# Kernel optimization log

Hardware: AMD Instinct MI355X
Metric: run time of the kernel (lower is better)

Reference implementation:

```python
import jax, jax.numpy as jnp
import numpy as np

B, P, DV, DT, E, A, K = 256, 192, 768, 768, 256, 8, 4


def _l2n(x):
    return x / jnp.maximum(jnp.linalg.norm(x, axis=-1, keepdims=True), 1e-12)


def _hungarian_min(cost):
    """Jonker-Volgenant style Hungarian (e-maxx formulation), minimizes cost.
    cost: [n, m] with n <= m. Returns (row_ind, col_ind) like scipy's
    linear_sum_assignment."""
    cost = np.asarray(cost, dtype=np.float64)
    n, m = cost.shape
    INF = 1e18
    u = np.zeros(n + 1)
    v = np.zeros(m + 1)
    p = np.zeros(m + 1, dtype=np.int64)   # p[j] = row matched to col j (1-based)
    way = np.zeros(m + 1, dtype=np.int64)
    for i in range(1, n + 1):
        p[0] = i
        j0 = 0
        minv = np.full(m + 1, INF)
        used = np.zeros(m + 1, dtype=bool)
        while True:
            used[j0] = True
            i0 = p[j0]
            cur = cost[i0 - 1] - u[i0] - v[1:]
            free = ~used[1:]
            better = free & (cur < minv[1:])
            minv[1:][better] = cur[better]
            way[1:][better] = j0
            cand = np.where(free, minv[1:], INF)
            j1 = int(np.argmin(cand)) + 1
            delta = cand[j1 - 1]
            u[p[used]] += delta
            v[used] -= delta
            minv[1:][free] -= delta
            j0 = j1
            if p[j0] == 0:
                break
        while j0 != 0:
            j1 = way[j0]
            p[j0] = p[j1]
            j0 = j1
    rows = p[1:]
    cols = np.arange(m)
    sel = rows != 0
    rows = rows[sel] - 1
    cols = cols[sel]
    order = np.argsort(rows)
    return rows[order], cols[order]


def _topk_assign_indices(sim_np, k):
    """Replicates get_topk_assign_similarity's iterative masked re-assignment,
    returning per-round match indices. sim_np: [B, A, P] numpy."""
    b_, a_, _ = sim_np.shape
    rows = np.zeros((k, b_, a_), dtype=np.int64)
    cols = np.zeros((k, b_, a_), dtype=np.int64)
    for b in range(b_):
        mat = sim_np[b].copy()
        for r in range(k):
            ri, ci = _hungarian_min(-mat)  # maximize similarity
            rows[r, b] = ri
            cols[r, b] = ci
            mat[ri, ci] = -100.0
        # (host loop over small per-sample Hungarian solves; this is exactly
        #  the serialized pattern the original module exhibits)
    return rows, cols


def setup_inputs() -> dict:
    key = jax.random.key(0)
    ks = jax.random.split(key, 8)
    s = (2.0 / E) ** 0.5  # kaiming_normal fan_out on [E, in] torch weight
    return {
        "visual_feature": jax.random.normal(ks[0], (B, 1 + P, DV), jnp.float32),
        "textual_feature": jax.random.normal(ks[1], (B, DT), jnp.float32),
        "attribute_feature": jax.random.normal(ks[2], (B * A, DT), jnp.float32),
        "att_nums": jnp.full((B,), A, dtype=jnp.int32),
        "Wv": jax.random.normal(ks[3], (DV, E), jnp.float32) * s,
        "bv": jnp.zeros((E,), jnp.float32),
        "Wt": jax.random.normal(ks[4], (DT, E), jnp.float32) * s,
        "bt": jnp.zeros((E,), jnp.float32),
        "Wp": jax.random.normal(ks[5], (DV, E), jnp.float32) * s,
        "bp": jnp.zeros((E,), jnp.float32),
        "Wa": jax.random.normal(ks[6], (DT, E), jnp.float32) * s,
        "ba": jnp.zeros((E,), jnp.float32),
    }


def reference(visual_feature, textual_feature, attribute_feature, att_nums,
              Wv, bv, Wt, bt, Wp, bp, Wa, ba):
    # ViT path: avgpool is None; split CLS token / patch tokens
    visual_embed = visual_feature[:, 0] @ Wv + bv            # [B, E]
    textual_embed = textual_feature @ Wt + bt                # [B, E]
    patch_embed = visual_feature[:, 1:] @ Wp + bp            # [B, P, E]
    att_embed = attribute_feature @ Wa + ba                  # [B*A, E]

    # get_local_similarity: L2-normalize then per-sample sim matrices.
    # att_nums is constant A per sample, so the ragged slicing is a reshape.
    att = _l2n(att_embed).reshape(B, A, E)
    pat = _l2n(patch_embed)
    sim = jnp.einsum('bae,bpe->bap', att, pat)               # [B, A, P]

    # Hungarian assignment on detached values (torch: .detach().cpu())
    rows, cols = _topk_assign_indices(np.asarray(sim), K)
    rows = jnp.asarray(rows)
    cols = jnp.asarray(cols)

    bidx = jnp.arange(B)[:, None]
    sim_m = sim
    total = jnp.zeros((B,), sim.dtype)
    for r in range(K):
        total = total + sim_m[bidx, rows[r], cols[r]].mean(-1)
        sim_m = sim_m.at[bidx, rows[r], cols[r]].set(-100.0)
    local_similarity = total / K                              # [B]

    return (visual_embed, textual_embed, local_similarity)
```

## Files before the change

### kernel.cpp

```cpp
#include <hip/hip_runtime.h>
#include <hip/hip_bf16.h>

typedef float f32x4 __attribute__((ext_vector_type(4)));
typedef short s16x8 __attribute__((ext_vector_type(8)));

__device__ __forceinline__ unsigned short f2bf(float f) {
  unsigned int x = __builtin_bit_cast(unsigned int, f);
  x += 0x7fffu + ((x >> 16) & 1u);
  return (unsigned short)(x >> 16);
}
__device__ __forceinline__ float bf2f(unsigned short u) {
  return __builtin_bit_cast(float, ((unsigned int)u) << 16);
}
__device__ __forceinline__ unsigned int packbf(float lo, float hi) {
  return (unsigned int)f2bf(lo) | ((unsigned int)f2bf(hi) << 16);
}
__device__ __forceinline__ void mfma16(f32x4& acc, s16x8 a, s16x8 b) {
  asm volatile("v_mfma_f32_16x16x32_bf16 %0, %1, %2, %0"
               : "+v"(acc)
               : "v"(a), "v"(b));
}
__device__ __forceinline__ void gload_lds16(const void* g, void* l) {
  __builtin_amdgcn_global_load_lds(
      (const __attribute__((address_space(1))) unsigned int*)g,
      (__attribute__((address_space(3))) unsigned int*)l, 16, 0, 0);
}

__global__ __launch_bounds__(256) void prep_wt(const float* __restrict__ W,
                                               unsigned short* __restrict__ Wt) {
  int i = blockIdx.x * 256 + threadIdx.x;
  int k = i >> 8, col = i & 255;
  int kt = k >> 5, kl = k & 31;
  unsigned off = (unsigned)((col * 64 + kl * 2) ^ ((col & 3) << 4));
  Wt[(unsigned)(kt * 16384 + off) >> 1] = f2bf(W[i]);
}

__global__ __launch_bounds__(512, 2) void patch_gemm(
    const float* __restrict__ vf, const unsigned short* __restrict__ Wt,
    const float* __restrict__ bias, unsigned short* __restrict__ patch) {
  __shared__ char lds[57344];
  __shared__ float rssq[192];

  const int tid = threadIdx.x;
  const int lane = tid & 63, wid = tid >> 6;
  const int wm = wid >> 2, wn = wid & 3;
  const int l15 = lane & 15, l4 = lane >> 4;
  const int blk = blockIdx.x;

  if (tid < 192) rssq[tid] = 0.f;

  const float* Ag = vf + ((size_t)blk * 193 + 1) * 768;

  f32x4 acc[6][4] = {};
  f32x4 areg[3];

  auto stageA_load = [&](int kt) {
#pragma unroll
    for (int c = 0; c < 3; ++c) {
      int idx4 = c * 512 + tid;
      int row = idx4 >> 3, k4 = (idx4 & 7) * 4;
      areg[c] = *(const f32x4*)(Ag + (size_t)row * 768 + kt * 32 + k4);
    }
  };
  auto stageA_write = [&](int buf) {
#pragma unroll
    for (int c = 0; c < 3; ++c) {
      int idx4 = c * 512 + tid;
      int row = idx4 >> 3, k4 = (idx4 & 7) * 4;
      unsigned off = (unsigned)((row * 64 + k4 * 2) ^ ((row & 3) << 4));
      uint2 u;
      u.x = packbf(areg[c].x, areg[c].y);
      u.y = packbf(areg[c].z, areg[c].w);
      *(uint2*)(lds + buf * 12288 + off) = u;
    }
  };
  auto stageB = [&](int kt, int buf) {
#pragma unroll
    for (int it = 0; it < 2; ++it) {
      int off = wid * 2048 + it * 1024;
      gload_lds16((const char*)Wt + kt * 16384 + off + lane * 16,
                  lds + 24576 + buf * 16384 + off);
    }
  };
  auto compute = [&](int buf) {
    const char* Ab = lds + buf * 12288;
    const char* Bb = lds + 24576 + buf * 16384;
    const int kb = l4 * 16;
    s16x8 af[6];
#pragma unroll
    for (int mf = 0; mf < 6; ++mf) {
      int row = wm * 96 + mf * 16 + l15;
      unsigned off = (unsigned)((row * 64 + kb) ^ ((row & 3) << 4));
      af[mf] = *(const s16x8*)(Ab + off);
    }
    s16x8 bfr[4];
#pragma unroll
    for (int nf = 0; nf < 4; ++nf) {
      int col = wn * 64 + nf * 16 + l15;
      unsigned off = (unsigned)((col * 64 + kb) ^ ((col & 3) << 4));
      bfr[nf] = *(const s16x8*)(Bb + off);
    }
#pragma unroll
    for (int mf = 0; mf < 6; ++mf)
#pragma unroll
      for (int nf = 0; nf < 4; ++nf) mfma16(acc[mf][nf], af[mf], bfr[nf]);
  };

  stageA_load(0);
  stageB(0, 0);
  stageA_write(0);
  __syncthreads();

  int cur = 0;
  for (int kt = 0; kt < 24; ++kt) {
    if (kt < 23) {
      stageA_load(kt + 1);
      stageB(kt + 1, cur ^ 1);
    }
    compute(cur);
    if (kt < 23) stageA_write(cur ^ 1);
    __syncthreads();
    cur ^= 1;
  }

  __builtin_amdgcn_sched_barrier(0);
  asm volatile("s_nop 7\n\ts_nop 7");
  __builtin_amdgcn_sched_barrier(0);

  float bcol[4];
#pragma unroll
  for (int nf = 0; nf < 4; ++nf) bcol[nf] = bias[wn * 64 + nf * 16 + l15];
#pragma unroll
  for (int mf = 0; mf < 6; ++mf)
#pragma unroll
    for (int nf = 0; nf < 4; ++nf)
#pragma unroll
      for (int j = 0; j < 4; ++j) acc[mf][nf][j] += bcol[nf];

#pragma unroll
  for (int mf = 0; mf < 6; ++mf)
#pragma unroll
    for (int j = 0; j < 4; ++j) {
      float p = 0.f;
#pragma unroll
      for (int nf = 0; nf < 4; ++nf) {
        float v = acc[mf][nf][j];
        p += v * v;
      }
#pragma unroll
      for (int m = 1; m < 16; m <<= 1) p += __shfl_xor(p, m);
      if (l15 == 0) atomicAdd(&rssq[wm * 96 + mf * 16 + l4 * 4 + j], p);
    }
  __syncthreads();

  unsigned short* outp = patch + (size_t)blk * 192 * 256;
#pragma unroll
  for (int mf = 0; mf < 6; ++mf)
#pragma unroll
    for (int j = 0; j < 4; ++j) {
      int row = wm * 96 + mf * 16 + l4 * 4 + j;
      float scale = 1.f / fmaxf(sqrtf(rssq[row]), 1e-12f);
#pragma unroll
      for (int nf = 0; nf < 4; ++nf) {
        int col = wn * 64 + nf * 16 + l15;
        outp[(size_t)row * 256 + col] = f2bf(acc[mf][nf][j] * scale);
      }
    }
}

template <int MODE>
__device__ __forceinline__ const float* row_ptr(const float* A, int r) {
  if constexpr (MODE == 0) {
    return A + (size_t)r * 768;
  } else {
    return A + (size_t)r * (193 * 768);
  }
}

template <int MODE>
__global__ __launch_bounds__(256) void small_gemm(
    const float* __restrict__ A, const float* __restrict__ W,
    const float* __restrict__ bias, float* __restrict__ C) {
  __shared__ float As[32][33];
  __shared__ float Bs[32][68];
  const int tid = threadIdx.x;
  const int row0 = blockIdx.y * 32, col0 = blockIdx.x * 64;
  const int tx = tid & 15, ty = tid >> 4;
  const int lr = tid >> 3, lk = (tid & 7) * 4;
  const float* Arow = row_ptr<MODE>(A, row0 + lr);
  const int bk = tid >> 4, bn = (tid & 15) * 4;
  const float* Wp = W + (size_t)bk * 256 + col0 + bn;
  float acc[2][4] = {};

  for (int k0 = 0; k0 < 768; k0 += 32) {
    float4 a0 = *(const float4*)(Arow + k0 + lk);
    float4 b0 = *(const float4*)(Wp + (size_t)k0 * 256);
    float4 b1 = *(const float4*)(Wp + (size_t)(k0 + 16) * 256);
    __syncthreads();
    As[lk + 0][lr] = a0.x; As[lk + 1][lr] = a0.y;
    As[lk + 2][lr] = a0.z; As[lk + 3][lr] = a0.w;
    *(float4*)&Bs[bk][bn] = b0;
    *(float4*)&Bs[bk + 16][bn] = b1;
    __syncthreads();
#pragma unroll
    for (int k = 0; k < 32; ++k) {
      float a0v = As[k][ty * 2], a1v = As[k][ty * 2 + 1];
      float4 bv = *(const float4*)&Bs[k][tx * 4];
      acc[0][0] += a0v * bv.x; acc[0][1] += a0v * bv.y;
      acc[0][2] += a0v * bv.z; acc[0][3] += a0v * bv.w;
      acc[1][0] += a1v * bv.x; acc[1][1] += a1v * bv.y;
      acc[1][2] += a1v * bv.z; acc[1][3] += a1v * bv.w;
    }
  }
  float4 b4 = *(const float4*)(bias + col0 + tx * 4);
#pragma unroll
  for (int i = 0; i < 2; ++i) {
    int r = row0 + ty * 2 + i;
    float4 o;
    o.x = acc[i][0] + b4.x; o.y = acc[i][1] + b4.y;
    o.z = acc[i][2] + b4.z; o.w = acc[i][3] + b4.w;
    *(float4*)(C + (size_t)r * 256 + col0 + tx * 4) = o;
  }
}

__global__ __launch_bounds__(256) void l2norm_kernel(float* __restrict__ X,
                                                     int rows) {
  int row = blockIdx.x * 4 + (threadIdx.x >> 6);
  int lane = threadIdx.x & 63;
  if (row >= rows) return;
  float4* px = (float4*)(X + (size_t)row * 256);
  float4 v = px[lane];
  float ss = v.x * v.x + v.y * v.y + v.z * v.z + v.w * v.w;
#pragma unroll
  for (int off = 1; off < 64; off <<= 1) ss += __shfl_xor(ss, off);
  float n = fmaxf(sqrtf(ss), 1e-12f);
  v.x /= n; v.y /= n; v.z /= n; v.w /= n;
  px[lane] = v;
}

__global__ __launch_bounds__(192) void sim_kernel(
    const float* __restrict__ att, const unsigned short* __restrict__ pat,
    float* __restrict__ sim) {
  const int b = blockIdx.x;
  __shared__ float attS[8][256];
  const int tid = threadIdx.x;
  for (int idx = tid; idx < 2048; idx += 192)
    ((float*)attS)[idx] = att[(size_t)b * 2048 + idx];
  __syncthreads();

  const unsigned short* prow = pat + ((size_t)b * 192 + tid) * 256;
  float acc[8] = {};
  for (int e8 = 0; e8 < 32; ++e8) {
    uint4 pv = *(const uint4*)(prow + e8 * 8);
    float f[8];
    f[0] = bf2f((unsigned short)(pv.x & 0xffff)); f[1] = bf2f((unsigned short)(pv.x >> 16));
    f[2] = bf2f((unsigned short)(pv.y & 0xffff)); f[3] = bf2f((unsigned short)(pv.y >> 16));
    f[4] = bf2f((unsigned short)(pv.z & 0xffff)); f[5] = bf2f((unsigned short)(pv.z >> 16));
    f[6] = bf2f((unsigned short)(pv.w & 0xffff)); f[7] = bf2f((unsigned short)(pv.w >> 16));
#pragma unroll
    for (int a = 0; a < 8; ++a) {
      const float* ap = &attS[a][e8 * 8];
#pragma unroll
      for (int i = 0; i < 8; ++i) acc[a] += f[i] * ap[i];
    }
  }
#pragma unroll
  for (int a = 0; a < 8; ++a)
    sim[(size_t)b * 1536 + a * 192 + tid] = acc[a];
}

__global__ __launch_bounds__(64) void hungarian_kernel(
    const float* __restrict__ sim, float* __restrict__ out) {
  const int b = blockIdx.x;
  const int lane = threadIdx.x;
  __shared__ float S[8][192];
  __shared__ int p[193];
  __shared__ int way[193];
  __shared__ double u[9];

  const float* simb = sim + (size_t)b * 1536;
  for (int idx = lane; idx < 1536; idx += 64) ((float*)S)[idx] = simb[idx];
  __syncthreads();

  const int j_0 = 1 + lane;
  const int j_1 = 65 + lane;
  const int j_2 = 129 + lane;

  double total = 0.0;

  for (int round = 0; round < 4; ++round) {
    for (int idx = lane; idx < 193; idx += 64) p[idx] = 0;
    if (lane < 9) u[lane] = 0.0;
    double v0 = 0.0, v1 = 0.0, v2 = 0.0;
    __syncthreads();

    for (int i = 1; i <= 8; ++i) {
      if (lane == 0) p[0] = i;
      double m0 = 1e18, m1 = 1e18, m2 = 1e18;
      int used = 0;
      int j0 = 0;
      __syncthreads();

      while (true) {
        if (j0 != 0 && ((j0 - 1) & 63) == lane) used |= 1 << ((j0 - 1) >> 6);
        const int i0 = p[j0];
        const double ui0 = u[i0];
        const float* Srow = S[i0 - 1];

        double bestv = 1e18;
        int bestj = 0x7fffffff;
        if (!(used & 1)) {
          double cur = -(double)Srow[j_0 - 1] - ui0 - v0;
          if (cur < m0) { m0 = cur; way[j_0] = j0; }
          if (m0 < bestv) { bestv = m0; bestj = j_0; }
        }
        if (!(used & 2)) {
          double cur = -(double)Srow[j_1 - 1] - ui0 - v1;
          if (cur < m1) { m1 = cur; way[j_1] = j0; }
          if (m1 < bestv) { bestv = m1; bestj = j_1; }
        }
        if (!(used & 4)) {
          double cur = -(double)Srow[j_2 - 1] - ui0 - v2;
          if (cur < m2) { m2 = cur; way[j_2] = j0; }
          if (m2 < bestv) { bestv = m2; bestj = j_2; }
        }
#pragma unroll
        for (int off = 1; off < 64; off <<= 1) {
          double ov = __shfl_xor(bestv, off);
          int oj = __shfl_xor(bestj, off);
          if (ov < bestv || (ov == bestv && oj < bestj)) {
            bestv = ov; bestj = oj;
          }
        }
        const double delta = bestv;
        const int j1 = bestj;

        if (lane == 0) u[i] += delta;
        if (used & 1) { v0 -= delta; int pj = p[j_0]; u[pj] += delta; } else m0 -= delta;
        if (used & 2) { v1 -= delta; int pj = p[j_1]; u[pj] += delta; } else m1 -= delta;
        if (used & 4) { v2 -= delta; int pj = p[j_2]; u[pj] += delta; } else m2 -= delta;
        __syncthreads();

        j0 = j1;
        if (p[j0] == 0) break;
      }

      if (lane == 0) {
        int j = j0;
        while (j != 0) {
          int jp = way[j];
          p[j] = p[jp];
          j = jp;
        }
      }
      __syncthreads();
    }

    double s = 0.0;
    {
      int pj = p[j_0];
      if (pj) { s += (double)S[pj - 1][j_0 - 1]; S[pj - 1][j_0 - 1] = -100.0f; }
      pj = p[j_1];
      if (pj) { s += (double)S[pj - 1][j_1 - 1]; S[pj - 1][j_1 - 1] = -100.0f; }
      pj = p[j_2];
      if (pj) { s += (double)S[pj - 1][j_2 - 1]; S[pj - 1][j_2 - 1] = -100.0f; }
    }
#pragma unroll
    for (int off = 1; off < 64; off <<= 1) s += __shfl_xor(s, off);
    total += s;
    __syncthreads();
  }

  if (lane == 0) out[b] = (float)(total * (1.0 / 32.0));
}

extern "C" void kernel_launch(void* const* d_in, const int* in_sizes, int n_in,
                              void* d_out, int out_size, void* d_ws,
                              size_t ws_size, hipStream_t stream) {
  const float* vf = (const float*)d_in[0];
  const float* tf = (const float*)d_in[1];
  const float* af = (const float*)d_in[2];
  const float* Wv = (const float*)d_in[4];
  const float* bv = (const float*)d_in[5];
  const float* Wt_w = (const float*)d_in[6];
  const float* bt = (const float*)d_in[7];
  const float* Wp = (const float*)d_in[8];
  const float* bp = (const float*)d_in[9];
  const float* Wa = (const float*)d_in[10];
  const float* ba = (const float*)d_in[11];

  float* out = (float*)d_out;
  float* visual_out = out;
  float* textual_out = out + 65536;
  float* ls_out = out + 131072;

  char* ws = (char*)d_ws;
  unsigned short* patch = (unsigned short*)ws;
  float* attE = (float*)(ws + (size_t)25165824);
  float* sim = (float*)(ws + (size_t)25165824 + 2097152);
  unsigned short* Wt_s = (unsigned short*)(ws + (size_t)25165824 + 2097152 + 1572864);

  prep_wt<<<768, 256, 0, stream>>>(Wp, Wt_s);

  small_gemm<1><<<dim3(4, 8), 256, 0, stream>>>(vf, Wv, bv, visual_out);
  small_gemm<0><<<dim3(4, 8), 256, 0, stream>>>(tf, Wt_w, bt, textual_out);
  small_gemm<0><<<dim3(4, 64), 256, 0, stream>>>(af, Wa, ba, attE);

  patch_gemm<<<256, 512, 0, stream>>>(vf, Wt_s, bp, patch);

  l2norm_kernel<<<512, 256, 0, stream>>>(attE, 2048);

  sim_kernel<<<256, 192, 0, stream>>>(attE, patch, sim);

  hungarian_kernel<<<256, 64, 0, stream>>>(sim, ls_out);
}
```

Before: 417.1 us.

## Keep Hungarian state in registers and drop per-iteration barriers

The Hungarian kernel now holds the similarity matrix, row potentials u, and column assignments in registers instead of LDS. The augmenting-path loop no longer needs a __syncthreads per step, because the next row index travels through the argmin shuffle reduction. Separately, the visual and textual GEMMs are merged into one launch and the l2norm launch is moved earlier. The intent is to cut LDS traffic, barrier latency and launch overhead in the serial Hungarian loop, at the cost of more registers and select chains.

```diff
diff --git a/kernel.cpp b/kernel.cpp
--- a/kernel.cpp
+++ b/kernel.cpp
@@ -168,17 +168,62 @@
     }
 }
 
-template <int MODE>
-__device__ __forceinline__ const float* row_ptr(const float* A, int r) {
-  if constexpr (MODE == 0) {
-    return A + (size_t)r * 768;
-  } else {
-    return A + (size_t)r * (193 * 768);
-  }
-}
-
-template <int MODE>
-__global__ __launch_bounds__(256) void small_gemm(
+__global__ __launch_bounds__(256) void vt_gemm(
+    const float* __restrict__ vf, const float* __restrict__ tf,
+    const float* __restrict__ Wv, const float* __restrict__ bv,
+    const float* __restrict__ Wtx, const float* __restrict__ bt,
+    float* __restrict__ out) {
+  __shared__ float As[32][33];
+  __shared__ float Bs[32][68];
+  const bool vis = blockIdx.y < 8;
+  const int row0 = (vis ? blockIdx.y : blockIdx.y - 8) * 32;
+  const int col0 = blockIdx.x * 64;
+  const float* A = vis ? vf : tf;
+  const float* W = vis ? Wv : Wtx;
+  const float* bias = vis ? bv : bt;
+  float* C = vis ? out : out + 65536;
+  const size_t rstride = vis ? (size_t)193 * 768 : (size_t)768;
+
+  const int tid = threadIdx.x;
+  const int tx = tid & 15, ty = tid >> 4;
+  const int lr = tid >> 3, lk = (tid & 7) * 4;
+  const float* Arow = A + (size_t)(row0 + lr) * rstride;
+  const int bk = tid >> 4, bn = (tid & 15) * 4;
+  const float* Wp = W + (size_t)bk * 256 + col0 + bn;
+  float acc[2][4] = {};
+
+  for (int k0 = 0; k0 < 768; k0 += 32) {
+    float4 a0 = *(const float4*)(Arow + k0 + lk);
+    float4 b0 = *(const float4*)(Wp + (size_t)k0 * 256);
+    float4 b1 = *(const float4*)(Wp + (size_t)(k0 + 16) * 256);
+    __syncthreads();
+    As[lk + 0][lr] = a0.x; As[lk + 1][lr] = a0.y;
+    As[lk + 2][lr] = a0.z; As[lk + 3][lr] = a0.w;
+    *(float4*)&Bs[bk][bn] = b0;
+    *(float4*)&Bs[bk + 16][bn] = b1;
+    __syncthreads();
+#pragma unroll
+    for (int k = 0; k < 32; ++k) {
+      float a0v = As[k][ty * 2], a1v = As[k][ty * 2 + 1];
+      float4 bv4 = *(const float4*)&Bs[k][tx * 4];
+      acc[0][0] += a0v * bv4.x; acc[0][1] += a0v * bv4.y;
+      acc[0][2] += a0v * bv4.z; acc[0][3] += a0v * bv4.w;
+      acc[1][0] += a1v * bv4.x; acc[1][1] += a1v * bv4.y;
+      acc[1][2] += a1v * bv4.z; acc[1][3] += a1v * bv4.w;
+    }
+  }
+  float4 b4 = *(const float4*)(bias + col0 + tx * 4);
+#pragma unroll
+  for (int i = 0; i < 2; ++i) {
+    int r = row0 + ty * 2 + i;
+    float4 o;
+    o.x = acc[i][0] + b4.x; o.y = acc[i][1] + b4.y;
+    o.z = acc[i][2] + b4.z; o.w = acc[i][3] + b4.w;
+    *(float4*)(C + (size_t)r * 256 + col0 + tx * 4) = o;
+  }
+}
+
+__global__ __launch_bounds__(256) void att_gemm(
     const float* __restrict__ A, const float* __restrict__ W,
     const float* __restrict__ bias, float* __restrict__ C) {
   __shared__ float As[32][33];
@@ -187,7 +232,7 @@
   const int row0 = blockIdx.y * 32, col0 = blockIdx.x * 64;
   const int tx = tid & 15, ty = tid >> 4;
   const int lr = tid >> 3, lk = (tid & 7) * 4;
-  const float* Arow = row_ptr<MODE>(A, row0 + lr);
+  const float* Arow = A + (size_t)(row0 + lr) * 768;
   const int bk = tid >> 4, bn = (tid & 15) * 4;
   const float* Wp = W + (size_t)bk * 256 + col0 + bn;
   float acc[2][4] = {};
@@ -205,11 +250,11 @@
 #pragma unroll
     for (int k = 0; k < 32; ++k) {
       float a0v = As[k][ty * 2], a1v = As[k][ty * 2 + 1];
-      float4 bv = *(const float4*)&Bs[k][tx * 4];
-      acc[0][0] += a0v * bv.x; acc[0][1] += a0v * bv.y;
-      acc[0][2] += a0v * bv.z; acc[0][3] += a0v * bv.w;
-      acc[1][0] += a1v * bv.x; acc[1][1] += a1v * bv.y;
-      acc[1][2] += a1v * bv.z; acc[1][3] += a1v * bv.w;
+      float4 bv4 = *(const float4*)&Bs[k][tx * 4];
+      acc[0][0] += a0v * bv4.x; acc[0][1] += a0v * bv4.y;
+      acc[0][2] += a0v * bv4.z; acc[0][3] += a0v * bv4.w;
+      acc[1][0] += a1v * bv4.x; acc[1][1] += a1v * bv4.y;
+      acc[1][2] += a1v * bv4.z; acc[1][3] += a1v * bv4.w;
     }
   }
   float4 b4 = *(const float4*)(bias + col0 + tx * 4);
@@ -273,25 +318,23 @@
     const float* __restrict__ sim, float* __restrict__ out) {
   const int b = blockIdx.x;
   const int lane = threadIdx.x;
-  __shared__ float S[8][192];
   __shared__ int p[193];
   __shared__ int way[193];
-  __shared__ double u[9];
-
+
+  float Sr[8][3];
   const float* simb = sim + (size_t)b * 1536;
-  for (int idx = lane; idx < 1536; idx += 64) ((float*)S)[idx] = simb[idx];
-  __syncthreads();
-
-  const int j_0 = 1 + lane;
-  const int j_1 = 65 + lane;
-  const int j_2 = 129 + lane;
+#pragma unroll
+  for (int r = 0; r < 8; ++r)
+#pragma unroll
+    for (int c = 0; c < 3; ++c) Sr[r][c] = simb[r * 192 + c * 64 + lane];
 
   double total = 0.0;
 
   for (int round = 0; round < 4; ++round) {
     for (int idx = lane; idx < 193; idx += 64) p[idx] = 0;
-    if (lane < 9) u[lane] = 0.0;
+    double u1 = 0, u2 = 0, u3 = 0, u4 = 0, u5 = 0, u6 = 0, u7 = 0, u8 = 0;
     double v0 = 0.0, v1 = 0.0, v2 = 0.0;
+    int pc0 = 0, pc1 = 0, pc2 = 0;
     __syncthreads();
 
     for (int i = 1; i <= 8; ++i) {
@@ -299,52 +342,75 @@
       double m0 = 1e18, m1 = 1e18, m2 = 1e18;
       int used = 0;
       int j0 = 0;
-      __syncthreads();
+      int pj0 = i;
+      int rowmask = 0;
 
       while (true) {
+        rowmask |= 1 << pj0;
         if (j0 != 0 && ((j0 - 1) & 63) == lane) used |= 1 << ((j0 - 1) >> 6);
-        const int i0 = p[j0];
-        const double ui0 = u[i0];
-        const float* Srow = S[i0 - 1];
+        const int i0 = __builtin_amdgcn_readfirstlane(pj0);
+
+        double ui0 = u1;
+        if (i0 == 2) ui0 = u2;
+        if (i0 == 3) ui0 = u3;
+        if (i0 == 4) ui0 = u4;
+        if (i0 == 5) ui0 = u5;
+        if (i0 == 6) ui0 = u6;
+        if (i0 == 7) ui0 = u7;
+        if (i0 == 8) ui0 = u8;
+
+        float s0 = Sr[0][0], s1 = Sr[0][1], s2 = Sr[0][2];
+#pragma unroll
+        for (int r = 1; r < 8; ++r)
+          if (i0 == r + 1) { s0 = Sr[r][0]; s1 = Sr[r][1]; s2 = Sr[r][2]; }
 
         double bestv = 1e18;
         int bestj = 0x7fffffff;
+        int bestpj = 0;
         if (!(used & 1)) {
-          double cur = -(double)Srow[j_0 - 1] - ui0 - v0;
-          if (cur < m0) { m0 = cur; way[j_0] = j0; }
-          if (m0 < bestv) { bestv = m0; bestj = j_0; }
+          double cur = -(double)s0 - ui0 - v0;
+          if (cur < m0) { m0 = cur; way[1 + lane] = j0; }
+          if (m0 < bestv) { bestv = m0; bestj = 1 + lane; bestpj = pc0; }
         }
         if (!(used & 2)) {
-          double cur = -(double)Srow[j_1 - 1] - ui0 - v1;
-          if (cur < m1) { m1 = cur; way[j_1] = j0; }
-          if (m1 < bestv) { bestv = m1; bestj = j_1; }
+          double cur = -(double)s1 - ui0 - v1;
+          if (cur < m1) { m1 = cur; way[65 + lane] = j0; }
+          if (m1 < bestv) { bestv = m1; bestj = 65 + lane; bestpj = pc1; }
         }
         if (!(used & 4)) {
-          double cur = -(double)Srow[j_2 - 1] - ui0 - v2;
-          if (cur < m2) { m2 = cur; way[j_2] = j0; }
-          if (m2 < bestv) { bestv = m2; bestj = j_2; }
+          double cur = -(double)s2 - ui0 - v2;
+          if (cur < m2) { m2 = cur; way[129 + lane] = j0; }
+          if (m2 < bestv) { bestv = m2; bestj = 129 + lane; bestpj = pc2; }
         }
 #pragma unroll
         for (int off = 1; off < 64; off <<= 1) {
           double ov = __shfl_xor(bestv, off);
           int oj = __shfl_xor(bestj, off);
+          int opj = __shfl_xor(bestpj, off);
           if (ov < bestv || (ov == bestv && oj < bestj)) {
-            bestv = ov; bestj = oj;
+            bestv = ov; bestj = oj; bestpj = opj;
           }
         }
         const double delta = bestv;
-        const int j1 = bestj;
-
-        if (lane == 0) u[i] += delta;
-        if (used & 1) { v0 -= delta; int pj = p[j_0]; u[pj] += delta; } else m0 -= delta;
-        if (used & 2) { v1 -= delta; int pj = p[j_1]; u[pj] += delta; } else m1 -= delta;
-        if (used & 4) { v2 -= delta; int pj = p[j_2]; u[pj] += delta; } else m2 -= delta;
-        __syncthreads();
-
-        j0 = j1;
-        if (p[j0] == 0) break;
+
+        if (rowmask & (1 << 1)) u1 += delta;
+        if (rowmask & (1 << 2)) u2 += delta;
+        if (rowmask & (1 << 3)) u3 += delta;
+        if (rowmask & (1 << 4)) u4 += delta;
+        if (rowmask & (1 << 5)) u5 += delta;
+        if (rowmask & (1 << 6)) u6 += delta;
+        if (rowmask & (1 << 7)) u7 += delta;
+        if (rowmask & (1 << 8)) u8 += delta;
+        if (used & 1) v0 -= delta; else m0 -= delta;
+        if (used & 2) v1 -= delta; else m1 -= delta;
+        if (used & 4) v2 -= delta; else m2 -= delta;
+
+        j0 = bestj;
+        pj0 = bestpj;
+        if (pj0 == 0) break;
       }
 
+      __syncthreads();
       if (lane == 0) {
         int j = j0;
         while (j != 0) {
@@ -354,16 +420,26 @@
         }
       }
       __syncthreads();
+      pc0 = p[1 + lane];
+      pc1 = p[65 + lane];
+      pc2 = p[129 + lane];
     }
 
     double s = 0.0;
-    {
-      int pj = p[j_0];
-      if (pj) { s += (double)S[pj - 1][j_0 - 1]; S[pj - 1][j_0 - 1] = -100.0f; }
-      pj = p[j_1];
-      if (pj) { s += (double)S[pj - 1][j_1 - 1]; S[pj - 1][j_1 - 1] = -100.0f; }
-      pj = p[j_2];
-      if (pj) { s += (double)S[pj - 1][j_2 - 1]; S[pj - 1][j_2 - 1] = -100.0f; }
+    if (pc0) {
+#pragma unroll
+      for (int r = 0; r < 8; ++r)
+        if (pc0 == r + 1) { s += (double)Sr[r][0]; Sr[r][0] = -100.f; }
+    }
+    if (pc1) {
+#pragma unroll
+      for (int r = 0; r < 8; ++r)
+        if (pc1 == r + 1) { s += (double)Sr[r][1]; Sr[r][1] = -100.f; }
+    }
+    if (pc2) {
+#pragma unroll
+      for (int r = 0; r < 8; ++r)
+        if (pc2 == r + 1) { s += (double)Sr[r][2]; Sr[r][2] = -100.f; }
     }
 #pragma unroll
     for (int off = 1; off < 64; off <<= 1) s += __shfl_xor(s, off);
@@ -382,7 +458,7 @@
   const float* af = (const float*)d_in[2];
   const float* Wv = (const float*)d_in[4];
   const float* bv = (const float*)d_in[5];
-  const float* Wt_w = (const float*)d_in[6];
+  const float* Wtx = (const float*)d_in[6];
   const float* bt = (const float*)d_in[7];
   const float* Wp = (const float*)d_in[8];
   const float* bp = (const float*)d_in[9];
@@ -391,7 +467,6 @@
 
   float* out = (float*)d_out;
   float* visual_out = out;
-  float* textual_out = out + 65536;
   float* ls_out = out + 131072;
 
   char* ws = (char*)d_ws;
@@ -402,14 +477,14 @@
 
   prep_wt<<<768, 256, 0, stream>>>(Wp, Wt_s);
 
-  small_gemm<1><<<dim3(4, 8), 256, 0, stream>>>(vf, Wv, bv, visual_out);
-  small_gemm<0><<<dim3(4, 8), 256, 0, stream>>>(tf, Wt_w, bt, textual_out);
-  small_gemm<0><<<dim3(4, 64), 256, 0, stream>>>(af, Wa, ba, attE);
+  vt_gemm<<<dim3(4, 16), 256, 0, stream>>>(vf, tf, Wv, bv, Wtx, bt, visual_out);
+
+  att_gemm<<<dim3(4, 64), 256, 0, stream>>>(af, Wa, ba, attE);
+
+  l2norm_kernel<<<512, 256, 0, stream>>>(attE, 2048);
 
   patch_gemm<<<256, 512, 0, stream>>>(vf, Wt_s, bp, patch);
 
-  l2norm_kernel<<<512, 256, 0, stream>>>(attE, 2048);
-
   sim_kernel<<<256, 192, 0, stream>>>(attE, patch, sim);
 
   hungarian_kernel<<<256, 64, 0, stream>>>(sim, ls_out);
```

After: 384.1 us. 1.09x faster.
